# Kernel tuning notes

Measured on AMD Instinct MI355X. Metric: run time of the kernel, lower is better.

Reference implementation:

```python
import jax, jax.numpy as jnp
import numpy as np

EMBED = 512
HEADS = 8
HIDDEN = 4 * EMBED
EPS = 1e-5


def setup_inputs() -> dict:
    key = jax.random.key(0)
    ks = jax.random.split(key, 12)
    s = lambda fan_in: 1.0 / np.sqrt(fan_in)
    return {
        "x": jax.random.normal(ks[0], (4, 2048, EMBED), dtype=jnp.float32),
        "ln1_g": jnp.ones((EMBED,), jnp.float32),
        "ln1_b": jnp.zeros((EMBED,), jnp.float32),
        "qkv_w": jax.random.uniform(ks[1], (EMBED, 3 * EMBED), jnp.float32, -s(EMBED), s(EMBED)),
        "qkv_b": jax.random.uniform(ks[2], (3 * EMBED,), jnp.float32, -s(EMBED), s(EMBED)),
        "proj_w": jax.random.uniform(ks[3], (EMBED, EMBED), jnp.float32, -s(EMBED), s(EMBED)),
        "proj_b": jax.random.uniform(ks[4], (EMBED,), jnp.float32, -s(EMBED), s(EMBED)),
        "ln2_g": jnp.ones((EMBED,), jnp.float32),
        "ln2_b": jnp.zeros((EMBED,), jnp.float32),
        "fc1_w": jax.random.uniform(ks[5], (EMBED, HIDDEN), jnp.float32, -s(EMBED), s(EMBED)),
        "fc1_b": jax.random.uniform(ks[6], (HIDDEN,), jnp.float32, -s(EMBED), s(EMBED)),
        "fc2_w": jax.random.uniform(ks[7], (HIDDEN, EMBED), jnp.float32, -s(HIDDEN), s(HIDDEN)),
        "fc2_b": jax.random.uniform(ks[8], (EMBED,), jnp.float32, -s(HIDDEN), s(HIDDEN)),
    }


def _layernorm(x, g, b):
    mu = jnp.mean(x, axis=-1, keepdims=True)
    var = jnp.mean(jnp.square(x - mu), axis=-1, keepdims=True)
    return (x - mu) * jax.lax.rsqrt(var + EPS) * g + b


def reference(x, ln1_g, ln1_b, qkv_w, qkv_b, proj_w, proj_b,
              ln2_g, ln2_b, fc1_w, fc1_b, fc2_w, fc2_b):
    B, N, C = x.shape
    H, D = HEADS, C // HEADS
    scale = D ** -0.5

    # --- attention sub-block (pre-LN) ---
    h = _layernorm(x, ln1_g, ln1_b)
    qkv = h @ qkv_w + qkv_b                      # [B,N,3C]
    q, k, v = jnp.split(qkv, 3, axis=-1)
    q = q.reshape(B, N, H, D).transpose(0, 2, 1, 3)  # [B,H,N,D]
    k = k.reshape(B, N, H, D).transpose(0, 2, 1, 3)
    v = v.reshape(B, N, H, D).transpose(0, 2, 1, 3)
    attn = jnp.einsum('bhqd,bhkd->bhqk', q, k) * scale
    attn = jax.nn.softmax(attn, axis=-1)
    o = jnp.einsum('bhqk,bhkd->bhqd', attn, v)
    o = o.transpose(0, 2, 1, 3).reshape(B, N, C)
    x = x + (o @ proj_w + proj_b)

    # --- MLP sub-block (pre-LN, exact GELU) ---
    h = _layernorm(x, ln2_g, ln2_b)
    h = jax.nn.gelu(h @ fc1_w + fc1_b, approximate=False)
    x = x + (h @ fc2_w + fc2_b)
    return x
```

## Files before the change

### kernel.cpp

```cpp
#include <hip/hip_runtime.h>
#include <math.h>


using bf16x8 = __attribute__((ext_vector_type(8))) short;
using f32x4  = __attribute__((ext_vector_type(4))) float;

typedef unsigned short u16;
typedef unsigned int   u32;

__device__ __forceinline__ u16 f2bf(float f) {
    u32 u; __builtin_memcpy(&u, &f, 4);
    u32 r = u + 0x7FFFu + ((u >> 16) & 1u);
    return (u16)(r >> 16);
}
__device__ __forceinline__ u32 fbits(float f) {
    u32 u; __builtin_memcpy(&u, &f, 4); return u;
}
__device__ __forceinline__ float f_from_bits(u32 u) {
    float f; __builtin_memcpy(&f, &u, 4); return f;
}
__device__ __forceinline__ u32 pack_trunc(float lo, float hi) {
    return __builtin_amdgcn_perm(fbits(hi), fbits(lo), 0x07060302u);
}
__device__ __forceinline__ void gload16(const void* g, void* l) {
    __builtin_amdgcn_global_load_lds(
        (const __attribute__((address_space(1))) unsigned int*)g,
        (__attribute__((address_space(3))) unsigned int*)l, 16, 0, 0);
}

__global__ __launch_bounds__(256) void k_pre(
        const float* __restrict__ w0, u16* __restrict__ d0,
        const float* __restrict__ w1, u16* __restrict__ d1,
        const float* __restrict__ w2, u16* __restrict__ d2,
        const float* __restrict__ w3, u16* __restrict__ d3,
        const float* __restrict__ x, const float* __restrict__ g,
        const float* __restrict__ bta, u16* __restrict__ hout) {
    __shared__ float tile[32][33];
    const int bid = blockIdx.x;
    if (bid < 3072) {
        const float* w; u16* dst; int K, N, tb;
        if (bid < 768)       { w = w0; dst = d0; K = 512;  N = 1536; tb = bid; }
        else if (bid < 1024) { w = w1; dst = d1; K = 512;  N = 512;  tb = bid - 768; }
        else if (bid < 2048) { w = w2; dst = d2; K = 512;  N = 2048; tb = bid - 1024; }
        else                 { w = w3; dst = d3; K = 2048; N = 512;  tb = bid - 2048; }
        const int nb = N >> 5;
        const int k0 = (tb / nb) << 5;
        const int n0 = (tb % nb) << 5;
        const int c = threadIdx.x & 31, r = threadIdx.x >> 5;
#pragma unroll
        for (int i = 0; i < 4; i++)
            tile[r + i * 8][c] = w[(size_t)(k0 + r + i * 8) * N + n0 + c];
        __syncthreads();
#pragma unroll
        for (int i = 0; i < 4; i++)
            dst[(size_t)(n0 + r + i * 8) * K + k0 + c] = f2bf(tile[c][r + i * 8]);
    } else {
        const int row  = ((bid - 3072) << 2) + (threadIdx.x >> 6);
        const int lane = threadIdx.x & 63;
        const float* xr = x + (size_t)row * 512 + lane * 8;
        float4 a = *(const float4*)xr;
        float4 c = *(const float4*)(xr + 4);
        float s = a.x + a.y + a.z + a.w + c.x + c.y + c.z + c.w;
        float q = a.x*a.x + a.y*a.y + a.z*a.z + a.w*a.w
                + c.x*c.x + c.y*c.y + c.z*c.z + c.w*c.w;
#pragma unroll
        for (int off = 32; off; off >>= 1) {
            s += __shfl_xor(s, off, 64);
            q += __shfl_xor(q, off, 64);
        }
        const float mean = s * (1.0f / 512.0f);
        const float var  = q * (1.0f / 512.0f) - mean * mean;
        const float rstd = rsqrtf(var + 1e-5f);
        float vv[8] = {a.x, a.y, a.z, a.w, c.x, c.y, c.z, c.w};
#pragma unroll
        for (int j = 0; j < 8; j++) {
            const int col = lane * 8 + j;
            hout[(size_t)row * 512 + col] = f2bf((vv[j] - mean) * rstd * g[col] + bta[col]);
        }
    }
}

__global__ __launch_bounds__(256) void k_ln(const float* __restrict__ x,
                                            const float* __restrict__ g,
                                            const float* __restrict__ bta,
                                            u16* __restrict__ out) {
    const int row  = (blockIdx.x << 2) + (threadIdx.x >> 6);
    const int lane = threadIdx.x & 63;
    const float* xr = x + (size_t)row * 512 + lane * 8;
    float4 a = *(const float4*)xr;
    float4 c = *(const float4*)(xr + 4);
    float s = a.x + a.y + a.z + a.w + c.x + c.y + c.z + c.w;
    float q = a.x*a.x + a.y*a.y + a.z*a.z + a.w*a.w
            + c.x*c.x + c.y*c.y + c.z*c.z + c.w*c.w;
#pragma unroll
    for (int off = 32; off; off >>= 1) {
        s += __shfl_xor(s, off, 64);
        q += __shfl_xor(q, off, 64);
    }
    const float mean = s * (1.0f / 512.0f);
    const float var  = q * (1.0f / 512.0f) - mean * mean;
    const float rstd = rsqrtf(var + 1e-5f);
    float vv[8] = {a.x, a.y, a.z, a.w, c.x, c.y, c.z, c.w};
#pragma unroll
    for (int j = 0; j < 8; j++) {
        const int col = lane * 8 + j;
        out[(size_t)row * 512 + col] = f2bf((vv[j] - mean) * rstd * g[col] + bta[col]);
    }
}

template <int EP, int TN>
__global__ __launch_bounds__(256, 3) void k_gemm(const u16* __restrict__ A,
                                                 const u16* __restrict__ Bt,
                                                 const float* __restrict__ bias,
                                                 const float* __restrict__ res,
                                                 float* __restrict__ outF,
                                                 u16* __restrict__ outB,
                                                 u16* __restrict__ out2,
                                                 int M, int N, int K) {
    constexpr int NT = TN / 32;
    __shared__ u16 As[128 * 64];
    __shared__ u16 Bs[TN * 64];
    const int nb = N / TN;
    const int xg = blockIdx.x & 7, sg = blockIdx.x >> 3;
    const int m0 = ((sg / nb) * 8 + xg) << 7;
    const int n0 = (sg % nb) * TN;
    const int t = threadIdx.x, lane = t & 63, w = t >> 6;
    const int wr = (w >> 1) << 6;
    const int wc = (w & 1) * (TN / 2);
    const int quad = lane >> 4, l15 = lane & 15;
    const int x7 = l15 & 7;

    f32x4 acc[4][NT];
#pragma unroll
    for (int i = 0; i < 4; i++)
#pragma unroll
        for (int j = 0; j < NT; j++) acc[i][j] = (f32x4){0.f, 0.f, 0.f, 0.f};

    const size_t Kb = (size_t)K * 2;
    const char* ga = (const char*)A + (size_t)m0 * Kb;
    const char* gb = (const char*)Bt + (size_t)n0 * Kb;
    const int o0 = t * 16;

    for (int k0 = 0; k0 < K; k0 += 64) {
        const int kb = k0 * 2;
#pragma unroll
        for (int i = 0; i < 4; i++) {
            const int o4 = i * 4096 + o0;
            const int row = o4 >> 7;
            const int lc = ((o4 >> 4) & 7) ^ (row & 7);
            gload16(ga + (size_t)row * Kb + kb + lc * 16, (char*)As + o4);
        }
#pragma unroll
        for (int i = 0; i < TN / 32; i++) {
            const int o4 = i * 4096 + o0;
            const int row = o4 >> 7;
            const int lc = ((o4 >> 4) & 7) ^ (row & 7);
            gload16(gb + (size_t)row * Kb + kb + lc * 16, (char*)Bs + o4);
        }
        __syncthreads();
#pragma unroll
        for (int ks = 0; ks < 2; ks++) {
            const int cidx = ((ks * 4 + quad) ^ x7) * 8;
            bf16x8 af[4], bfr[NT];
#pragma unroll
            for (int i = 0; i < 4; i++)
                af[i] = *(const bf16x8*)(As + (wr + i * 16 + l15) * 64 + cidx);
#pragma unroll
            for (int j = 0; j < NT; j++)
                bfr[j] = *(const bf16x8*)(Bs + (wc + j * 16 + l15) * 64 + cidx);
#pragma unroll
            for (int mt = 0; mt < 4; mt++)
#pragma unroll
                for (int nt = 0; nt < NT; nt++)
                    acc[mt][nt] = __builtin_amdgcn_mfma_f32_16x16x32_bf16(
                        af[mt], bfr[nt], acc[mt][nt], 0, 0, 0);
        }
        __syncthreads();
    }

    const bool vpart = (EP == 3) && (n0 >= 1024);
    const bool qpart = (EP == 3) && (n0 < 512);
#pragma unroll
    for (int mt = 0; mt < 4; mt++)
#pragma unroll
        for (int nt = 0; nt < NT; nt++) {
            const int col = n0 + wc + nt * 16 + l15;
            const float bi = bias[col];
            const int row0 = m0 + wr + mt * 16 + quad * 4;
            if (vpart) {
                const int b = row0 >> 11, key = row0 & 2047;
                const int hd = col - 1024;
                u32 p0 = (u32)f2bf(acc[mt][nt][0] + bi) |
                         ((u32)f2bf(acc[mt][nt][1] + bi) << 16);
                u32 p1 = (u32)f2bf(acc[mt][nt][2] + bi) |
                         ((u32)f2bf(acc[mt][nt][3] + bi) << 16);
                *(uint2*)(out2 + (size_t)(b * 512 + hd) * 2048 + key) = make_uint2(p0, p1);
            } else {
#pragma unroll
                for (int r = 0; r < 4; r++) {
                    const int row = row0 + r;
                    float v = acc[mt][nt][r] + bi;
                    const size_t oi = (size_t)row * N + col;
                    if (EP == 1) {
                        float y = v * (0.79788456f + 0.035677408f * v * v);
                        y = fminf(y, 40.0f);
                        float tE = exp2f(y * 2.88539008f);
                        v = v * tE * __builtin_amdgcn_rcpf(tE + 1.0f);
                    }
                    if (qpart) v *= 0.18033688f;
                    if (EP == 2) outF[oi] = v + res[oi];
                    else         outB[oi] = f2bf(v);
                }
            }
        }
}

__global__ __launch_bounds__(256, 4) void k_attn(const u16* __restrict__ qkv,
                                                 const u16* __restrict__ vt,
                                                 u16* __restrict__ po0,
                                                 u16* __restrict__ po1,
                                                 float* __restrict__ pden) {
    __shared__ u16 smem[20480];
    const int bid = blockIdx.x;
    const int h = bid & 7, sg = bid >> 3;
    const int qt = sg & 15, kh = (sg >> 4) & 1, b = sg >> 5;
    const int q0 = qt << 7;
    const int t = threadIdx.x, lane = t & 63, w = t >> 6;
    const int quad = lane >> 4, l15 = lane & 15;
    const int x7 = l15 & 7;

    char* sb = (char*)smem;
    const char* gk = (const char*)qkv + (size_t)((b << 11) + (kh << 10)) * 3072 + 1024 + h * 128;
    const char* gv = (const char*)vt + (size_t)((b << 3) + h) * 64 * 4096 + (kh << 10) * 2;

#pragma unroll
    for (int i = 0; i < 2; i++) {
        const int o4 = i * 4096 + t * 16;
        const int row = o4 >> 7;
        const int lc = ((o4 >> 4) & 7) ^ (row & 7);
        gload16(gk + (size_t)row * 3072 + lc * 16, sb + o4);
        gload16(gv + (size_t)row * 4096 + lc * 16, sb + 8192 + o4);
    }

    bf16x8 qf[2][2];
    {
        const u16* gqp = qkv + (size_t)((b << 11) + q0 + w * 32 + l15) * 1536 + h * 64;
#pragma unroll
        for (int ks = 0; ks < 2; ks++)
#pragma unroll
            for (int nt = 0; nt < 2; nt++)
                qf[ks][nt] = *(const bf16x8*)(gqp + (size_t)(nt * 16) * 1536 + (ks * 4 + quad) * 8);
    }

    f32x4 accO[4][2];
    float denp[2] = {0.f, 0.f};
#pragma unroll
    for (int mt = 0; mt < 4; mt++)
#pragma unroll
        for (int nt = 0; nt < 2; nt++) accO[mt][nt] = (f32x4){0.f, 0.f, 0.f, 0.f};

    u16* Pw = smem + 16384 + w * 1024;

    for (int kt = 0; kt < 16; kt++) {
        const int cur = kt & 1;
        __syncthreads();
        if (kt < 15) {
            const int kk2 = (kt + 1) << 6;
            char* db = sb + (cur ^ 1) * 16384;
#pragma unroll
            for (int i = 0; i < 2; i++) {
                const int o4 = i * 4096 + t * 16;
                const int row = o4 >> 7;
                const int lc = ((o4 >> 4) & 7) ^ (row & 7);
                gload16(gk + (size_t)(kk2 + row) * 3072 + lc * 16, db + o4);
                gload16(gv + (size_t)row * 4096 + (size_t)kk2 * 2 + lc * 16, db + 8192 + o4);
            }
        }
        const u16* Ksc = smem + cur * 8192;
        const u16* Vsc = Ksc + 4096;

        f32x4 s[4][2];
#pragma unroll
        for (int mt = 0; mt < 4; mt++)
#pragma unroll
            for (int nt = 0; nt < 2; nt++) s[mt][nt] = (f32x4){0.f, 0.f, 0.f, 0.f};
#pragma unroll
        for (int ks = 0; ks < 2; ks++) {
            const int cidx = ((ks * 4 + quad) ^ x7) * 8;
            bf16x8 kf[4];
#pragma unroll
            for (int mt = 0; mt < 4; mt++)
                kf[mt] = *(const bf16x8*)(Ksc + (mt * 16 + l15) * 64 + cidx);
            __builtin_amdgcn_s_setprio(1);
#pragma unroll
            for (int mt = 0; mt < 4; mt++)
#pragma unroll
                for (int nt = 0; nt < 2; nt++)
                    s[mt][nt] = __builtin_amdgcn_mfma_f32_16x16x32_bf16(
                        kf[mt], qf[ks][nt], s[mt][nt], 0, 0, 0);
            __builtin_amdgcn_s_setprio(0);
        }

        bf16x8 vf[2][4];
#pragma unroll
        for (int ks = 0; ks < 2; ks++) {
            const int cidx = ((ks * 4 + quad) ^ x7) * 8;
#pragma unroll
            for (int mt = 0; mt < 4; mt++)
                vf[ks][mt] = *(const bf16x8*)(Vsc + (mt * 16 + l15) * 64 + cidx);
        }

#pragma unroll
        for (int nt = 0; nt < 2; nt++) {
#pragma unroll
            for (int mt = 0; mt < 4; mt++) {
                const float p0 = __builtin_amdgcn_exp2f(s[mt][nt][0]);
                const float p1 = __builtin_amdgcn_exp2f(s[mt][nt][1]);
                const float p2 = __builtin_amdgcn_exp2f(s[mt][nt][2]);
                const float p3 = __builtin_amdgcn_exp2f(s[mt][nt][3]);
                denp[nt] += (p0 + p1) + (p2 + p3);
                const u32 d0 = pack_trunc(p0, p1);
                const u32 d1 = pack_trunc(p2, p3);
                const int pidx = l15 * 64 +
                                 (((2 * mt + (quad >> 1)) ^ x7) << 3) + (quad & 1) * 4;
                *(uint2*)(&Pw[pidx]) = make_uint2(d0, d1);
            }
#pragma unroll
            for (int ks = 0; ks < 2; ks++) {
                const int cidx = ((ks * 4 + quad) ^ x7) * 8;
                const bf16x8 pf = *(const bf16x8*)(Pw + l15 * 64 + cidx);
                __builtin_amdgcn_s_setprio(1);
#pragma unroll
                for (int mt = 0; mt < 4; mt++)
                    accO[mt][nt] = __builtin_amdgcn_mfma_f32_16x16x32_bf16(
                        vf[ks][mt], pf, accO[mt][nt], 0, 0, 0);
                __builtin_amdgcn_s_setprio(0);
            }
        }
    }

    u16* po = kh ? po1 : po0;
#pragma unroll
    for (int nt = 0; nt < 2; nt++) {
        float dn = denp[nt];
        dn += __shfl_xor(dn, 16, 64);
        dn += __shfl_xor(dn, 32, 64);
        if (quad == 0)
            pden[(size_t)(((kh << 5) + (b << 3) + h) << 11) + q0 + w * 32 + nt * 16 + l15] = dn;
#pragma unroll
        for (int mt = 0; mt < 4; mt++) {
            const int qg = q0 + w * 32 + nt * 16 + l15;
            const u32 p0 = (u32)f2bf(accO[mt][nt][0]) | ((u32)f2bf(accO[mt][nt][1]) << 16);
            const u32 p1 = (u32)f2bf(accO[mt][nt][2]) | ((u32)f2bf(accO[mt][nt][3]) << 16);
            *(uint2*)(po + (size_t)((b << 11) + qg) * 512 + h * 64 + mt * 16 + quad * 4) =
                make_uint2(p0, p1);
        }
    }
}

__global__ __launch_bounds__(256) void k_combine(u16* __restrict__ po0,
                                                 const u16* __restrict__ po1,
                                                 const float* __restrict__ pden) {
    const int idx8 = (blockIdx.x * 256 + threadIdx.x) * 8;
    const int row = idx8 >> 9, col = idx8 & 511;
    const int h = col >> 6, q = row & 2047, b = row >> 11;
    const size_t di = (size_t)(((b << 3) + h) << 11) + q;
    const float den = pden[di] + pden[di + (32 << 11)];
    const float r = __builtin_amdgcn_rcpf(den);
    uint4 a = *(const uint4*)(po0 + idx8);
    uint4 c = *(const uint4*)(po1 + idx8);
    u32 av[4] = {a.x, a.y, a.z, a.w}, cv[4] = {c.x, c.y, c.z, c.w}, ov[4];
#pragma unroll
    for (int i = 0; i < 4; i++) {
        const float lo = (f_from_bits(av[i] << 16) + f_from_bits(cv[i] << 16)) * r;
        const float hi = (f_from_bits(av[i] & 0xFFFF0000u) +
                          f_from_bits(cv[i] & 0xFFFF0000u)) * r;
        ov[i] = (u32)f2bf(lo) | ((u32)f2bf(hi) << 16);
    }
    *(uint4*)(po0 + idx8) = make_uint4(ov[0], ov[1], ov[2], ov[3]);
}

extern "C" void kernel_launch(void* const* d_in, const int* in_sizes, int n_in,
                              void* d_out, int out_size, void* d_ws, size_t ws_size,
                              hipStream_t stream) {
    const float* x      = (const float*)d_in[0];
    const float* ln1_g  = (const float*)d_in[1];
    const float* ln1_b  = (const float*)d_in[2];
    const float* qkv_w  = (const float*)d_in[3];
    const float* qkv_b  = (const float*)d_in[4];
    const float* proj_w = (const float*)d_in[5];
    const float* proj_b = (const float*)d_in[6];
    const float* ln2_g  = (const float*)d_in[7];
    const float* ln2_b  = (const float*)d_in[8];
    const float* fc1_w  = (const float*)d_in[9];
    const float* fc1_b  = (const float*)d_in[10];
    const float* fc2_w  = (const float*)d_in[11];
    const float* fc2_b  = (const float*)d_in[12];
    float* out = (float*)d_out;
    char* ws = (char*)d_ws;

    u16*   qkv_wT = (u16*)(ws + 0);
    u16*   proj_wT= (u16*)(ws + 1572864);
    u16*   fc1_wT = (u16*)(ws + 2097152);
    u16*   fc2_wT = (u16*)(ws + 4194304);
    u16*   h      = (u16*)(ws + 6291456);
    float* pden   = (float*)(ws + 6291456);
    u16*   qkv    = (u16*)(ws + 14680064);
    u16*   vt     = (u16*)(ws + 39845888);
    u16*   o      = (u16*)(ws + 48234496);
    u16*   po1    = (u16*)(ws + 56623104);
    float* x1     = (float*)(ws + 56623104);
    u16*   f1     = (u16*)(ws + 14680064);
    u16*   h2     = h;

    k_pre<<<5120, 256, 0, stream>>>(qkv_w, qkv_wT, proj_w, proj_wT,
                                    fc1_w, fc1_wT, fc2_w, fc2_wT,
                                    x, ln1_g, ln1_b, h);
    k_gemm<3,128><<<(8192/128)*(1536/128), 256, 0, stream>>>(
        h, qkv_wT, qkv_b, nullptr, nullptr, qkv, vt, 8192, 1536, 512);
    k_attn<<<1024, 256, 0, stream>>>(qkv, vt, o, po1, pden);
    k_combine<<<2048, 256, 0, stream>>>(o, po1, pden);
    k_gemm<2,64><<<(8192/128)*(512/64), 256, 0, stream>>>(
        o, proj_wT, proj_b, x, x1, nullptr, nullptr, 8192, 512, 512);
    k_ln<<<2048, 256, 0, stream>>>(x1, ln2_g, ln2_b, h2);
    k_gemm<1,128><<<(8192/128)*(2048/128), 256, 0, stream>>>(
        h2, fc1_wT, fc1_b, nullptr, nullptr, f1, nullptr, 8192, 2048, 512);
    k_gemm<2,64><<<(8192/128)*(512/64), 256, 0, stream>>>(
        f1, fc2_wT, fc2_b, x1, out, nullptr, nullptr, 8192, 512, 2048);
}
```

Measured before the change: 281.2 us.

## Switch attention to 32x32x16 MFMA and pass P through registers via permlane32_swap

Rewrites the attention kernel's inner loop to use 32x32x16 bf16 MFMA instead of 16x16x32 for both QK^T and PV. The probability tile is rearranged in registers with permlane32_swap instead of being written to and read back from a per-wave LDS scratch. This removes the P round-trip through shared memory and shrinks the LDS footprint. The trade-off is larger 16-wide accumulators, which raises register pressure, and a more complex lane mapping that must match the MFMA operand layout.

```diff
diff --git a/kernel.cpp b/kernel.cpp
--- a/kernel.cpp
+++ b/kernel.cpp
@@ -4,6 +4,7 @@
 
 using bf16x8 = __attribute__((ext_vector_type(8))) short;
 using f32x4  = __attribute__((ext_vector_type(4))) float;
+using f32x16 = __attribute__((ext_vector_type(16))) float;
 
 typedef unsigned short u16;
 typedef unsigned int   u32;
@@ -220,14 +221,14 @@
                                                  u16* __restrict__ po0,
                                                  u16* __restrict__ po1,
                                                  float* __restrict__ pden) {
-    __shared__ u16 smem[20480];
+    __shared__ u16 smem[16384];
     const int bid = blockIdx.x;
     const int h = bid & 7, sg = bid >> 3;
     const int qt = sg & 15, kh = (sg >> 4) & 1, b = sg >> 5;
     const int q0 = qt << 7;
     const int t = threadIdx.x, lane = t & 63, w = t >> 6;
-    const int quad = lane >> 4, l15 = lane & 15;
-    const int x7 = l15 & 7;
+    const int l31 = lane & 31, hi = lane >> 5;
+    const int x7 = l31 & 7;
 
     char* sb = (char*)smem;
     const char* gk = (const char*)qkv + (size_t)((b << 11) + (kh << 10)) * 3072 + 1024 + h * 128;
@@ -242,24 +243,18 @@
         gload16(gv + (size_t)row * 4096 + lc * 16, sb + 8192 + o4);
     }
 
-    bf16x8 qf[2][2];
+    bf16x8 qf[4];
     {
-        const u16* gqp = qkv + (size_t)((b << 11) + q0 + w * 32 + l15) * 1536 + h * 64;
-#pragma unroll
-        for (int ks = 0; ks < 2; ks++)
-#pragma unroll
-            for (int nt = 0; nt < 2; nt++)
-                qf[ks][nt] = *(const bf16x8*)(gqp + (size_t)(nt * 16) * 1536 + (ks * 4 + quad) * 8);
-    }
-
-    f32x4 accO[4][2];
-    float denp[2] = {0.f, 0.f};
-#pragma unroll
-    for (int mt = 0; mt < 4; mt++)
-#pragma unroll
-        for (int nt = 0; nt < 2; nt++) accO[mt][nt] = (f32x4){0.f, 0.f, 0.f, 0.f};
-
-    u16* Pw = smem + 16384 + w * 1024;
+        const u16* gqp = qkv + (size_t)((b << 11) + q0 + w * 32 + l31) * 1536 + h * 64 + hi * 8;
+#pragma unroll
+        for (int ks = 0; ks < 4; ks++)
+            qf[ks] = *(const bf16x8*)(gqp + ks * 16);
+    }
+
+    f32x16 accO[2];
+#pragma unroll
+    for (int i = 0; i < 16; i++) { accO[0][i] = 0.f; accO[1][i] = 0.f; }
+    float dn = 0.f;
 
     for (int kt = 0; kt < 16; kt++) {
         const int cur = kt & 1;
@@ -279,83 +274,79 @@
         const u16* Ksc = smem + cur * 8192;
         const u16* Vsc = Ksc + 4096;
 
-        f32x4 s[4][2];
-#pragma unroll
-        for (int mt = 0; mt < 4; mt++)
-#pragma unroll
-            for (int nt = 0; nt < 2; nt++) s[mt][nt] = (f32x4){0.f, 0.f, 0.f, 0.f};
-#pragma unroll
-        for (int ks = 0; ks < 2; ks++) {
-            const int cidx = ((ks * 4 + quad) ^ x7) * 8;
-            bf16x8 kf[4];
-#pragma unroll
-            for (int mt = 0; mt < 4; mt++)
-                kf[mt] = *(const bf16x8*)(Ksc + (mt * 16 + l15) * 64 + cidx);
+        f32x16 s2[2];
+#pragma unroll
+        for (int i = 0; i < 16; i++) { s2[0][i] = 0.f; s2[1][i] = 0.f; }
+#pragma unroll
+        for (int ks = 0; ks < 4; ks++) {
+            const int cx = ((ks * 2 + hi) ^ x7) * 8;
+            bf16x8 kf0 = *(const bf16x8*)(Ksc + l31 * 64 + cx);
+            bf16x8 kf1 = *(const bf16x8*)(Ksc + (32 + l31) * 64 + cx);
             __builtin_amdgcn_s_setprio(1);
-#pragma unroll
-            for (int mt = 0; mt < 4; mt++)
-#pragma unroll
-                for (int nt = 0; nt < 2; nt++)
-                    s[mt][nt] = __builtin_amdgcn_mfma_f32_16x16x32_bf16(
-                        kf[mt], qf[ks][nt], s[mt][nt], 0, 0, 0);
+            s2[0] = __builtin_amdgcn_mfma_f32_32x32x16_bf16(kf0, qf[ks], s2[0], 0, 0, 0);
+            s2[1] = __builtin_amdgcn_mfma_f32_32x32x16_bf16(kf1, qf[ks], s2[1], 0, 0, 0);
             __builtin_amdgcn_s_setprio(0);
         }
 
-        bf16x8 vf[2][4];
-#pragma unroll
-        for (int ks = 0; ks < 2; ks++) {
-            const int cidx = ((ks * 4 + quad) ^ x7) * 8;
-#pragma unroll
-            for (int mt = 0; mt < 4; mt++)
-                vf[ks][mt] = *(const bf16x8*)(Vsc + (mt * 16 + l15) * 64 + cidx);
-        }
-
-#pragma unroll
-        for (int nt = 0; nt < 2; nt++) {
-#pragma unroll
-            for (int mt = 0; mt < 4; mt++) {
-                const float p0 = __builtin_amdgcn_exp2f(s[mt][nt][0]);
-                const float p1 = __builtin_amdgcn_exp2f(s[mt][nt][1]);
-                const float p2 = __builtin_amdgcn_exp2f(s[mt][nt][2]);
-                const float p3 = __builtin_amdgcn_exp2f(s[mt][nt][3]);
-                denp[nt] += (p0 + p1) + (p2 + p3);
-                const u32 d0 = pack_trunc(p0, p1);
-                const u32 d1 = pack_trunc(p2, p3);
-                const int pidx = l15 * 64 +
-                                 (((2 * mt + (quad >> 1)) ^ x7) << 3) + (quad & 1) * 4;
-                *(uint2*)(&Pw[pidx]) = make_uint2(d0, d1);
+        u32 pfu[4][4];
+#pragma unroll
+        for (int mt = 0; mt < 2; mt++) {
+            float pv[16];
+#pragma unroll
+            for (int r = 0; r < 16; r++) {
+                pv[r] = __builtin_amdgcn_exp2f(s2[mt][r]);
+                dn += pv[r];
             }
-#pragma unroll
-            for (int ks = 0; ks < 2; ks++) {
-                const int cidx = ((ks * 4 + quad) ^ x7) * 8;
-                const bf16x8 pf = *(const bf16x8*)(Pw + l15 * 64 + cidx);
-                __builtin_amdgcn_s_setprio(1);
-#pragma unroll
-                for (int mt = 0; mt < 4; mt++)
-                    accO[mt][nt] = __builtin_amdgcn_mfma_f32_16x16x32_bf16(
-                        vf[ks][mt], pf, accO[mt][nt], 0, 0, 0);
-                __builtin_amdgcn_s_setprio(0);
-            }
+            u32 pk[4][2];
+#pragma unroll
+            for (int c = 0; c < 4; c++)
+#pragma unroll
+                for (int m = 0; m < 2; m++)
+                    pk[c][m] = pack_trunc(pv[4 * c + 2 * m], pv[4 * c + 2 * m + 1]);
+#pragma unroll
+            for (int ksl = 0; ksl < 2; ksl++)
+#pragma unroll
+                for (int m = 0; m < 2; m++) {
+                    auto rr = __builtin_amdgcn_permlane32_swap(
+                        pk[ksl * 2][m], pk[ksl * 2 + 1][m], false, false);
+                    pfu[mt * 2 + ksl][m]     = rr[0];
+                    pfu[mt * 2 + ksl][m + 2] = rr[1];
+                }
+        }
+        __builtin_amdgcn_sched_barrier(0);
+
+#pragma unroll
+        for (int ks = 0; ks < 4; ks++) {
+            u32 pw[4] = {pfu[ks][0], pfu[ks][1], pfu[ks][2], pfu[ks][3]};
+            bf16x8 pfv;
+            __builtin_memcpy(&pfv, pw, 16);
+            const int cx = ((ks * 2 + hi) ^ x7) * 8;
+            bf16x8 vf0 = *(const bf16x8*)(Vsc + l31 * 64 + cx);
+            bf16x8 vf1 = *(const bf16x8*)(Vsc + (32 + l31) * 64 + cx);
+            __builtin_amdgcn_s_setprio(1);
+            accO[0] = __builtin_amdgcn_mfma_f32_32x32x16_bf16(vf0, pfv, accO[0], 0, 0, 0);
+            accO[1] = __builtin_amdgcn_mfma_f32_32x32x16_bf16(vf1, pfv, accO[1], 0, 0, 0);
+            __builtin_amdgcn_s_setprio(0);
         }
     }
 
     u16* po = kh ? po1 : po0;
-#pragma unroll
-    for (int nt = 0; nt < 2; nt++) {
-        float dn = denp[nt];
-        dn += __shfl_xor(dn, 16, 64);
-        dn += __shfl_xor(dn, 32, 64);
-        if (quad == 0)
-            pden[(size_t)(((kh << 5) + (b << 3) + h) << 11) + q0 + w * 32 + nt * 16 + l15] = dn;
-#pragma unroll
-        for (int mt = 0; mt < 4; mt++) {
-            const int qg = q0 + w * 32 + nt * 16 + l15;
-            const u32 p0 = (u32)f2bf(accO[mt][nt][0]) | ((u32)f2bf(accO[mt][nt][1]) << 16);
-            const u32 p1 = (u32)f2bf(accO[mt][nt][2]) | ((u32)f2bf(accO[mt][nt][3]) << 16);
-            *(uint2*)(po + (size_t)((b << 11) + qg) * 512 + h * 64 + mt * 16 + quad * 4) =
+    dn += __shfl_xor(dn, 32, 64);
+    const int qg = q0 + w * 32 + l31;
+    if (hi == 0)
+        pden[(size_t)(((kh << 5) + (b << 3) + h) << 11) + qg] = dn;
+#pragma unroll
+    for (int mtd = 0; mtd < 2; mtd++)
+#pragma unroll
+        for (int g = 0; g < 4; g++) {
+            const u32 p0 = (u32)f2bf(accO[mtd][4 * g + 0]) |
+                           ((u32)f2bf(accO[mtd][4 * g + 1]) << 16);
+            const u32 p1 = (u32)f2bf(accO[mtd][4 * g + 2]) |
+                           ((u32)f2bf(accO[mtd][4 * g + 3]) << 16);
+            const int d0 = mtd * 32 + g * 8 + hi * 4;
+            *(uint2*)(po + (size_t)((b << 11) + qg) * 512 + h * 64 + d0) =
                 make_uint2(p0, p1);
         }
-    }
 }
 
 __global__ __launch_bounds__(256) void k_combine(u16* __restrict__ po0,
```

Result: faster. 244.0 us (-13.2%).
